# Performance work log

Hardware: AMD Instinct MI355X
Metric: run time of the kernel (lower is better)

Reference implementation:

```python
import jax, jax.numpy as jnp
import numpy as np

EPS = 1e-5
N_HEADS = 12


def _layernorm(x, scale, shift):
    mean = jnp.mean(x, axis=-1, keepdims=True)
    var = jnp.mean((x - mean) ** 2, axis=-1, keepdims=True)
    return scale * (x - mean) / jnp.sqrt(var + EPS) + shift


def setup_inputs() -> dict:
    key = jax.random.key(0)
    ks = jax.random.split(key, 8)
    B, L, D = 4, 1024, 768
    inp = {
        "x": jax.random.normal(ks[0], (B, L, D), jnp.float32),
        "Wq": jax.random.normal(ks[1], (D, D), jnp.float32) * 0.02,
        "Wk": jax.random.normal(ks[2], (D, D), jnp.float32) * 0.02,
        "Wv": jax.random.normal(ks[3], (D, D), jnp.float32) * 0.02,
        "Wo": jax.random.normal(ks[4], (D, D), jnp.float32) * 0.02,
        "bo": jnp.zeros((D,), jnp.float32),
        "scale1": jnp.ones((D,), jnp.float32),
        "shift1": jnp.zeros((D,), jnp.float32),
        "scale2": jnp.ones((D,), jnp.float32),
        "shift2": jnp.zeros((D,), jnp.float32),
        "centers": jax.random.normal(ks[5], (D, D), jnp.float32) * 0.1,  # [num_kernels=D, D]
        "lengthscale": jnp.ones((D,), jnp.float32),
        "Wf": jax.random.normal(ks[6], (D, D), jnp.float32) * 0.02,  # [num_kernels, D]
        "bf": jnp.zeros((D,), jnp.float32),
    }
    return inp


def reference(x, Wq, Wk, Wv, Wo, bo, scale1, shift1, scale2, shift2,
              centers, lengthscale, Wf, bf):
    B, L, D = x.shape
    H = N_HEADS
    hd = D // H

    # --- pre-norm causal MHA + residual ---
    h = _layernorm(x, scale1, shift1)
    q = (h @ Wq).reshape(B, L, H, hd).transpose(0, 2, 1, 3)  # [B,H,L,hd]
    k = (h @ Wk).reshape(B, L, H, hd).transpose(0, 2, 1, 3)
    v = (h @ Wv).reshape(B, L, H, hd).transpose(0, 2, 1, 3)

    scores = jnp.einsum("bhqd,bhkd->bhqk", q, k) / jnp.sqrt(jnp.float32(hd))
    causal = jnp.tril(jnp.ones((L, L), bool))
    scores = jnp.where(causal, scores, -jnp.inf)
    attn = jax.nn.softmax(scores, axis=-1)
    ctx = jnp.einsum("bhqk,bhkd->bhqd", attn, v).transpose(0, 2, 1, 3).reshape(B, L, D)
    x = x + (ctx @ Wo + bo)

    # --- pre-norm RBF-kernel FFN + residual ---
    h = _layernorm(x, scale2, shift2)
    hf = (h / lengthscale).reshape(B * L, D)          # ARD scaling
    cf = centers / lengthscale                        # [K, D]
    sq = (jnp.sum(hf * hf, -1)[:, None]
          + jnp.sum(cf * cf, -1)[None, :]
          - 2.0 * hf @ cf.T)
    K = jnp.exp(-0.5 * jnp.maximum(sq, 0.0))          # [B*L, K]
    ff = (K @ Wf + bf).reshape(B, L, D)
    return x + ff
```

## Files before the change

kernel.cpp:

```cpp
#include <hip/hip_runtime.h>

#define EPS_LN 1e-5f

constexpr int Dm   = 768;
constexpr int Bb   = 4;
constexpr int Ls   = 1024;
constexpr int Hh   = 12;
constexpr int HD   = 64;
constexpr int ROWS = Bb * Ls;
constexpr size_t S = (size_t)ROWS * Dm;
constexpr size_t WSZ = (size_t)Dm * Dm;

typedef __attribute__((ext_vector_type(8))) short bf16x8;
typedef __attribute__((ext_vector_type(4))) float f32x4;
typedef const __attribute__((address_space(1))) unsigned int* gas_p;
typedef __attribute__((address_space(3))) unsigned int* las_p;

__device__ __forceinline__ unsigned short f2bf(float f) {
  unsigned int u = __float_as_uint(f);
  u += 0x7fffu + ((u >> 16) & 1u);
  return (unsigned short)(u >> 16);
}
__device__ __forceinline__ void gl_lds16(const unsigned short* g, unsigned short* l) {
  __builtin_amdgcn_global_load_lds((gas_p)g, (las_p)l, 16, 0, 0);
}

__global__ void __launch_bounds__(256) prep_kernel(
    const float* __restrict__ W0, const float* __restrict__ W1,
    const float* __restrict__ W2, const float* __restrict__ W3,
    const float* __restrict__ W4, unsigned short* __restrict__ wtBase,
    const float* __restrict__ centers, const float* __restrict__ ls,
    unsigned short* __restrict__ cb, float* __restrict__ cn,
    const float* __restrict__ x, const float* __restrict__ scale,
    const float* __restrict__ shift, unsigned short* __restrict__ hb)
{
  __shared__ float smem[64 * 65];
  int bx = blockIdx.x, t = threadIdx.x;
  if (bx < 720) {
    int w = bx / 144, rem = bx - w * 144;
    int ky = rem / 12, nx = rem - ky * 12;
    const float* W = w == 0 ? W0 : w == 1 ? W1 : w == 2 ? W2 : w == 3 ? W3 : W4;
    unsigned short* WT = wtBase + (size_t)w * WSZ;
    int k0 = ky * 64, n0 = nx * 64;
    int c = t & 63, r4 = t >> 6;
    #pragma unroll
    for (int p = 0; p < 16; p++) {
      int r = p * 4 + r4;
      smem[r * 65 + c] = W[(size_t)(k0 + r) * Dm + n0 + c];
    }
    __syncthreads();
    #pragma unroll
    for (int p = 0; p < 16; p++) {
      int r = p * 4 + r4;
      WT[(size_t)(n0 + r) * Dm + k0 + c] = f2bf(smem[c * 65 + r]);
    }
  } else if (bx < 1488) {
    int j = bx - 720;
    float s = 0.f;
    #pragma unroll
    for (int i = 0; i < 3; i++) {
      int k = t + 256 * i;
      float c = centers[(size_t)j * Dm + k] / ls[k];
      cb[(size_t)j * Dm + k] = f2bf(c);
      s += c * c;
    }
    smem[t] = s; __syncthreads();
    for (int o = 128; o > 0; o >>= 1) { if (t < o) smem[t] += smem[t + o]; __syncthreads(); }
    if (t == 0) cn[j] = smem[0];
  } else {
    int row = bx - 1488;
    size_t base = (size_t)row * Dm;
    float v0 = x[base + t], v1 = x[base + t + 256], v2 = x[base + t + 512];
    smem[t] = v0 + v1 + v2; __syncthreads();
    for (int o = 128; o > 0; o >>= 1) { if (t < o) smem[t] += smem[t + o]; __syncthreads(); }
    float mean = smem[0] * (1.0f / Dm);
    __syncthreads();
    float d0 = v0 - mean, d1 = v1 - mean, d2 = v2 - mean;
    smem[t] = d0*d0 + d1*d1 + d2*d2; __syncthreads();
    for (int o = 128; o > 0; o >>= 1) { if (t < o) smem[t] += smem[t + o]; __syncthreads(); }
    float rstd = rsqrtf(smem[0] * (1.0f / Dm) + EPS_LN);
    float dd[3] = {d0, d1, d2};
    #pragma unroll
    for (int i = 0; i < 3; i++) {
      int c = t + 256 * i;
      hb[base + c] = f2bf(scale[c] * dd[i] * rstd + shift[c]);
    }
  }
}

__global__ void __launch_bounds__(256) ln2_kernel(
    const float* __restrict__ xin, const float* __restrict__ scale,
    const float* __restrict__ shift, const float* __restrict__ ls,
    unsigned short* __restrict__ o, float* __restrict__ hn)
{
  int row = blockIdx.x, t = threadIdx.x;
  __shared__ float red[256];
  size_t base = (size_t)row * Dm;
  float v0 = xin[base + t], v1 = xin[base + t + 256], v2 = xin[base + t + 512];
  red[t] = v0 + v1 + v2; __syncthreads();
  for (int oo = 128; oo > 0; oo >>= 1) { if (t < oo) red[t] += red[t + oo]; __syncthreads(); }
  float mean = red[0] * (1.0f / Dm);
  __syncthreads();
  float d0 = v0 - mean, d1 = v1 - mean, d2 = v2 - mean;
  red[t] = d0*d0 + d1*d1 + d2*d2; __syncthreads();
  for (int oo = 128; oo > 0; oo >>= 1) { if (t < oo) red[t] += red[t + oo]; __syncthreads(); }
  float rstd = rsqrtf(red[0] * (1.0f / Dm) + EPS_LN);
  float dd[3] = {d0, d1, d2};
  float hsum = 0.f;
  #pragma unroll
  for (int i = 0; i < 3; i++) {
    int c = t + 256 * i;
    float hv = (scale[c] * dd[i] * rstd + shift[c]) / ls[c];
    o[base + c] = f2bf(hv);
    hsum += hv * hv;
  }
  __syncthreads();
  red[t] = hsum; __syncthreads();
  for (int o2 = 128; o2 > 0; o2 >>= 1) { if (t < o2) red[t] += red[t + o2]; __syncthreads(); }
  if (t == 0) hn[row] = red[0];
}

__global__ void __launch_bounds__(256) gemm_qkv(
    const unsigned short* __restrict__ Abf,
    const unsigned short* __restrict__ wqT,
    const unsigned short* __restrict__ wkT,
    const unsigned short* __restrict__ wvT,
    unsigned short* __restrict__ qb,
    unsigned short* __restrict__ kb,
    unsigned short* __restrict__ vbt)
{
  int m0 = blockIdx.y * 64, n0 = blockIdx.x * 64;
  __shared__ unsigned short sm[4096 + 3 * 4096];
  int tid = threadIdx.x;
  int lane = tid & 63, wave = tid >> 6;
  int quad = lane >> 4, l15 = lane & 15;
  int wr = (wave >> 1) << 5, wc = (wave & 1) << 5;

  f32x4 acc[3][2][2];
  #pragma unroll
  for (int w = 0; w < 3; w++)
    #pragma unroll
    for (int i = 0; i < 2; i++)
      #pragma unroll
      for (int j = 0; j < 2; j++) acc[w][i][j] = (f32x4){0.f, 0.f, 0.f, 0.f};

  const unsigned short* gA = Abf + (size_t)(m0 + (tid >> 2)) * Dm + ((tid & 3) << 3);
  size_t bOff = (size_t)(n0 + (tid >> 2)) * Dm + ((tid & 3) << 3);
  const unsigned short* gB[3] = { wqT + bOff, wkT + bOff, wvT + bOff };

  union Frag { bf16x8 v; ushort4 h[2]; };

  for (int k0 = 0; k0 < Dm; k0 += 64) {
    gl_lds16(gA + k0,      &sm[tid * 8]);
    gl_lds16(gA + k0 + 32, &sm[2048 + tid * 8]);
    #pragma unroll
    for (int w = 0; w < 3; w++) {
      gl_lds16(gB[w] + k0,      &sm[4096 + w * 4096 + tid * 8]);
      gl_lds16(gB[w] + k0 + 32, &sm[4096 + w * 4096 + 2048 + tid * 8]);
    }
    __syncthreads();
    Frag af[2][2];
    #pragma unroll
    for (int kc = 0; kc < 2; kc++)
      #pragma unroll
      for (int mi = 0; mi < 2; mi++)
        af[kc][mi].v = *(const bf16x8*)&sm[kc * 2048 + (wr + mi * 16 + l15) * 32 + quad * 8];
    #pragma unroll
    for (int w = 0; w < 3; w++)
      #pragma unroll
      for (int kc = 0; kc < 2; kc++)
        #pragma unroll
        for (int ni = 0; ni < 2; ni++) {
          Frag bf;
          bf.v = *(const bf16x8*)&sm[4096 + w * 4096 + kc * 2048 + (wc + ni * 16 + l15) * 32 + quad * 8];
          #pragma unroll
          for (int mi = 0; mi < 2; mi++)
            acc[w][mi][ni] = __builtin_amdgcn_mfma_f32_16x16x32_bf16(
                af[kc][mi].v, bf.v, acc[w][mi][ni], 0, 0, 0);
        }
    __syncthreads();
  }

  #pragma unroll
  for (int w = 0; w < 2; w++) {
    unsigned short* ob = w ? kb : qb;
    #pragma unroll
    for (int mi = 0; mi < 2; mi++)
      #pragma unroll
      for (int ni = 0; ni < 2; ni++)
        #pragma unroll
        for (int rg = 0; rg < 4; rg++) {
          int gr = m0 + wr + mi * 16 + quad * 4 + rg;
          int gc = n0 + wc + ni * 16 + l15;
          ob[(size_t)gr * Dm + gc] = f2bf(acc[w][mi][ni][rg]);
        }
  }
  #pragma unroll
  for (int mi = 0; mi < 2; mi++)
    #pragma unroll
    for (int ni = 0; ni < 2; ni++)
      #pragma unroll
      for (int rg = 0; rg < 4; rg++) {
        int rl = wr + mi * 16 + quad * 4 + rg;
        int cl = wc + ni * 16 + l15;
        sm[cl * 72 + rl] = f2bf(acc[2][mi][ni][rg]);
      }
  __syncthreads();
  {
    int d = tid >> 2, c0 = (tid & 3) * 16;
    int b_ = m0 >> 10, keybase = m0 & 1023;
    unsigned short* dst = vbt + ((size_t)((blockIdx.x * 4 + b_) * 64 + d)) * 1024 + keybase + c0;
    #pragma unroll
    for (int i = 0; i < 16; i += 4)
      *(ushort4*)(dst + i) = *(const ushort4*)&sm[d * 72 + c0 + i];
  }
}

template<int MODE>
__global__ void __launch_bounds__(256) gemm64(
    const unsigned short* __restrict__ Abf,
    const unsigned short* __restrict__ BT,
    unsigned short* __restrict__ o0,
    float* __restrict__ outF,
    const float* __restrict__ residF,
    const float* __restrict__ biasF,
    const float* __restrict__ hn,
    const float* __restrict__ cn)
{
  __shared__ unsigned short Asm[2][2048];
  __shared__ unsigned short Bsm[2][2048];
  int tid = threadIdx.x;
  int m0 = blockIdx.y * 64, n0 = blockIdx.x * 64;

  if (MODE >= 2) {
    __shared__ float r2[256];
    float mn = 1e30f;
    for (int i = tid; i < ROWS; i += 256) mn = fminf(mn, hn[i]);
    r2[tid] = mn; __syncthreads();
    for (int o = 128; o > 0; o >>= 1) { if (tid < o) r2[tid] = fminf(r2[tid], r2[tid + o]); __syncthreads(); }
    float hmin = r2[0];
    __syncthreads();
    float mx = 0.f;
    for (int i = tid; i < Dm; i += 256) mx = fmaxf(mx, cn[i]);
    r2[tid] = mx; __syncthreads();
    for (int o = 128; o > 0; o >>= 1) { if (tid < o) r2[tid] = fmaxf(r2[tid], r2[tid + o]); __syncthreads(); }
    float cmax = r2[0];
    float a = sqrtf(hmin), bq = sqrtf(cmax);
    bool allz = (a > bq) && ((a - bq) * (a - bq) > 300.0f);
    if (allz) {
      if (MODE == 2) return;
      int r = m0 + (tid >> 2), c0 = n0 + (tid & 3) * 16;
      size_t idx = (size_t)r * Dm + c0;
      #pragma unroll
      for (int i = 0; i < 16; i += 4) {
        float4 xv = *(const float4*)(residF + idx + i);
        float4 ov;
        ov.x = xv.x + biasF[c0 + i + 0];
        ov.y = xv.y + biasF[c0 + i + 1];
        ov.z = xv.z + biasF[c0 + i + 2];
        ov.w = xv.w + biasF[c0 + i + 3];
        *(float4*)(outF + idx + i) = ov;
      }
      return;
    }
    __syncthreads();
  }

  int lane = tid & 63, wave = tid >> 6;
  int quad = lane >> 4, l15 = lane & 15;
  int wr = (wave >> 1) << 5, wc = (wave & 1) << 5;

  f32x4 acc[2][2];
  #pragma unroll
  for (int i = 0; i < 2; i++)
    #pragma unroll
    for (int j = 0; j < 2; j++) acc[i][j] = (f32x4){0.f, 0.f, 0.f, 0.f};

  const unsigned short* gA = Abf + (size_t)(m0 + (tid >> 2)) * Dm + ((tid & 3) << 3);
  const unsigned short* gB = BT  + (size_t)(n0 + (tid >> 2)) * Dm + ((tid & 3) << 3);

  union Frag { bf16x8 v; ushort4 h[2]; };

  for (int k0 = 0; k0 < Dm; k0 += 64) {
    gl_lds16(gA + k0,      &Asm[0][tid * 8]);
    gl_lds16(gA + k0 + 32, &Asm[1][tid * 8]);
    gl_lds16(gB + k0,      &Bsm[0][tid * 8]);
    gl_lds16(gB + k0 + 32, &Bsm[1][tid * 8]);
    __syncthreads();
    #pragma unroll
    for (int kc = 0; kc < 2; kc++) {
      Frag af[2], bfb[2];
      #pragma unroll
      for (int i = 0; i < 2; i++) {
        af[i].v  = *(const bf16x8*)&Asm[kc][(wr + i * 16 + l15) * 32 + quad * 8];
        bfb[i].v = *(const bf16x8*)&Bsm[kc][(wc + i * 16 + l15) * 32 + quad * 8];
      }
      #pragma unroll
      for (int mi = 0; mi < 2; mi++)
        #pragma unroll
        for (int ni = 0; ni < 2; ni++)
          acc[mi][ni] = __builtin_amdgcn_mfma_f32_16x16x32_bf16(
              af[mi].v, bfb[ni].v, acc[mi][ni], 0, 0, 0);
    }
    __syncthreads();
  }

  #pragma unroll
  for (int mi = 0; mi < 2; mi++)
    #pragma unroll
    for (int ni = 0; ni < 2; ni++)
      #pragma unroll
      for (int rg = 0; rg < 4; rg++) {
        int gr = m0 + wr + mi * 16 + quad * 4 + rg;
        int gc = n0 + wc + ni * 16 + l15;
        size_t idx = (size_t)gr * Dm + gc;
        float v = acc[mi][ni][rg];
        if (MODE == 2) {
          float sq = fmaxf(hn[gr] + cn[gc] - 2.0f * v, 0.f);
          o0[idx] = f2bf(__expf(-0.5f * sq));
        } else {
          outF[idx] = residF[idx] + v + biasF[gc];
        }
      }
}

__global__ void __launch_bounds__(256) attn_flash(
    const unsigned short* __restrict__ q,
    const unsigned short* __restrict__ k,
    const unsigned short* __restrict__ vbt,
    unsigned short* __restrict__ ctx)
{
  int bx = blockIdx.x;
  int qt = (bx & 1) ? (15 - (bx >> 1)) : (bx >> 1);
  int h  = blockIdx.y;
  int b  = blockIdx.z;
  int tid = threadIdx.x;
  int lane = tid & 63, wave = tid >> 6;
  int quad = lane >> 4, l15 = lane & 15;

  __shared__ unsigned short Ks[2][2048];
  __shared__ unsigned short Vt[2][2048];
  __shared__ unsigned short QP[4608];

  size_t baseQK = (size_t)(b * Ls) * Dm + h * HD;
  const unsigned short* gVt = vbt + (size_t)((h * 4 + b) * 64 + (tid >> 2)) * 1024 + ((tid & 3) << 3);

  {
    const unsigned short* gQ = q + baseQK + (size_t)(qt * 64 + (tid >> 2)) * Dm + ((tid & 3) << 3);
    gl_lds16(gQ,      &QP[tid * 8]);
    gl_lds16(gQ + 32, &QP[2048 + tid * 8]);
  }
  __syncthreads();

  union Frag { bf16x8 v; ushort4 h[2]; };
  Frag afq[2];
  #pragma unroll
  for (int kc = 0; kc < 2; kc++)
    afq[kc].v = *(const bf16x8*)&QP[kc * 2048 + (wave * 16 + l15) * 32 + quad * 8];

  f32x4 O[4];
  #pragma unroll
  for (int nj = 0; nj < 4; nj++) O[nj] = (f32x4){0.f, 0.f, 0.f, 0.f};
  float lsum[4] = {0.f, 0.f, 0.f, 0.f};

  const unsigned short* gK = k + baseQK + (size_t)(tid >> 2) * Dm + ((tid & 3) << 3);

  for (int kt = 0; kt <= qt; kt++) {
    gl_lds16(gK + (size_t)(kt * 64) * Dm,      &Ks[0][tid * 8]);
    gl_lds16(gK + (size_t)(kt * 64) * Dm + 32, &Ks[1][tid * 8]);
    gl_lds16(gVt + kt * 64,      &Vt[0][tid * 8]);
    gl_lds16(gVt + kt * 64 + 32, &Vt[1][tid * 8]);
    __syncthreads();

    f32x4 sacc[4];
    #pragma unroll
    for (int ni = 0; ni < 4; ni++) {
      sacc[ni] = (f32x4){0.f, 0.f, 0.f, 0.f};
      #pragma unroll
      for (int kc = 0; kc < 2; kc++) {
        Frag bk;
        bk.v = *(const bf16x8*)&Ks[kc][(ni * 16 + l15) * 32 + quad * 8];
        sacc[ni] = __builtin_amdgcn_mfma_f32_16x16x32_bf16(afq[kc].v, bk.v, sacc[ni], 0, 0, 0);
      }
    }

    if (kt == qt) {
      #pragma unroll
      for (int ni = 0; ni < 4; ni++)
        #pragma unroll
        for (int rg = 0; rg < 4; rg++) {
          int rowl = wave * 16 + quad * 4 + rg;
          int coll = ni * 16 + l15;
          if (coll > rowl) sacc[ni][rg] = -1e30f;
        }
    }

    unsigned short (*Ps)[72] = (unsigned short(*)[72])QP;
    #pragma unroll
    for (int ni = 0; ni < 4; ni++)
      #pragma unroll
      for (int rg = 0; rg < 4; rg++) {
        float p = __expf(sacc[ni][rg] * 0.125f);
        lsum[rg] += p;
        Ps[wave * 16 + quad * 4 + rg][ni * 16 + l15] = f2bf(p);
      }

    Frag ap[2];
    #pragma unroll
    for (int kc = 0; kc < 2; kc++)
      ap[kc].v = *(const bf16x8*)&Ps[wave * 16 + l15][kc * 32 + quad * 8];

    #pragma unroll
    for (int nj = 0; nj < 4; nj++)
      #pragma unroll
      for (int kc = 0; kc < 2; kc++) {
        Frag bv;
        bv.v = *(const bf16x8*)&Vt[kc][(nj * 16 + l15) * 32 + quad * 8];
        O[nj] = __builtin_amdgcn_mfma_f32_16x16x32_bf16(ap[kc].v, bv.v, O[nj], 0, 0, 0);
      }
    __syncthreads();
  }

  float linv[4];
  #pragma unroll
  for (int rg = 0; rg < 4; rg++) {
    float l = lsum[rg];
    #pragma unroll
    for (int m = 1; m < 16; m <<= 1) l += __shfl_xor(l, m, 16);
    linv[rg] = 1.0f / l;
  }
  #pragma unroll
  for (int nj = 0; nj < 4; nj++)
    #pragma unroll
    for (int rg = 0; rg < 4; rg++) {
      int row = qt * 64 + wave * 16 + quad * 4 + rg;
      int col = nj * 16 + l15;
      ctx[baseQK + (size_t)row * Dm + col] = f2bf(O[nj][rg] * linv[rg]);
    }
}

extern "C" void kernel_launch(void* const* d_in, const int* in_sizes, int n_in,
                              void* d_out, int out_size, void* d_ws, size_t ws_size,
                              hipStream_t stream)
{
  const float* x      = (const float*)d_in[0];
  const float* Wq     = (const float*)d_in[1];
  const float* Wk     = (const float*)d_in[2];
  const float* Wv     = (const float*)d_in[3];
  const float* Wo     = (const float*)d_in[4];
  const float* bo     = (const float*)d_in[5];
  const float* scale1 = (const float*)d_in[6];
  const float* shift1 = (const float*)d_in[7];
  const float* scale2 = (const float*)d_in[8];
  const float* shift2 = (const float*)d_in[9];
  const float* centers= (const float*)d_in[10];
  const float* lsp    = (const float*)d_in[11];
  const float* Wf     = (const float*)d_in[12];
  const float* bfv    = (const float*)d_in[13];
  float* out = (float*)d_out;

  unsigned short* wsu = (unsigned short*)d_ws;
  unsigned short* wqT = wsu;
  unsigned short* wkT = wsu + WSZ;
  unsigned short* wvT = wsu + 2 * WSZ;
  unsigned short* woT = wsu + 3 * WSZ;
  unsigned short* wfT = wsu + 4 * WSZ;
  unsigned short* cb  = wsu + 5 * WSZ;
  unsigned short* bufA = wsu + 6 * WSZ;
  unsigned short* bufB = bufA + S;
  unsigned short* hb  = bufA;
  unsigned short* qb  = bufB;
  unsigned short* kb  = bufB + S;
  unsigned short* vbt = bufB + 2 * S;
  unsigned short* ctx = bufA;
  float* x1f          = (float*)bufB;
  unsigned short* hf  = bufB + 2 * S;
  unsigned short* Km  = bufA;
  float* hn = (float*)(bufB + 3 * S);
  float* cn = hn + ROWS;

  dim3 gg(Dm / 64, ROWS / 64);

  prep_kernel<<<5584, 256, 0, stream>>>(Wq, Wk, Wv, Wo, Wf, wsu,
                                        centers, lsp, cb, cn,
                                        x, scale1, shift1, hb);
  gemm_qkv<<<dim3(12, 64), 256, 0, stream>>>(hb, wqT, wkT, wvT, qb, kb, vbt);
  attn_flash<<<dim3(Ls / 64, Hh, Bb), 256, 0, stream>>>(qb, kb, vbt, ctx);
  gemm64<1><<<gg, 256, 0, stream>>>(ctx, woT, nullptr, x1f, x, bo, nullptr, nullptr);
  ln2_kernel<<<ROWS, 256, 0, stream>>>(x1f, scale2, shift2, lsp, hf, hn);
  gemm64<2><<<gg, 256, 0, stream>>>(hf, cb, Km, nullptr, nullptr, nullptr, hn, cn);
  gemm64<3><<<gg, 256, 0, stream>>>(Km, wfT, nullptr, out, x1f, bfv, hn, cn);
}
```

Measured before the change: 190.0 us.

## Use 128x128 MFMA tiles for QKV and output-projection GEMMs

```diff
diff --git a/kernel.cpp b/kernel.cpp
--- a/kernel.cpp
+++ b/kernel.cpp
@@ -120,100 +120,141 @@
   if (t == 0) hn[row] = red[0];
 }
 
-__global__ void __launch_bounds__(256) gemm_qkv(
+__device__ __forceinline__ void gemm128_loop(
     const unsigned short* __restrict__ Abf,
-    const unsigned short* __restrict__ wqT,
-    const unsigned short* __restrict__ wkT,
-    const unsigned short* __restrict__ wvT,
+    const unsigned short* __restrict__ BT,
+    unsigned short* sm, int m0, int n0, int tid, f32x4 (&acc)[4][4])
+{
+  int lane = tid & 63, wave = tid >> 6;
+  int quad = lane >> 4, l15 = lane & 15;
+  int wr = (wave >> 1) << 6, wc = (wave & 1) << 6;
+
+  const unsigned short* gA = Abf + (size_t)(m0 + (tid >> 3)) * Dm + ((tid & 7) << 3);
+  const unsigned short* gB = BT  + (size_t)(n0 + (tid >> 3)) * Dm + ((tid & 7) << 3);
+
+  for (int k0 = 0; k0 < Dm; k0 += 64) {
+    #pragma unroll
+    for (int r = 0; r < 4; r++) {
+      gl_lds16(gA + (size_t)(r * 32) * Dm + k0, &sm[r * 2048 + tid * 8]);
+      gl_lds16(gB + (size_t)(r * 32) * Dm + k0, &sm[8192 + r * 2048 + tid * 8]);
+    }
+    __syncthreads();
+    #pragma unroll
+    for (int kc = 0; kc < 2; kc++) {
+      bf16x8 af[4], bfv[4];
+      #pragma unroll
+      for (int i = 0; i < 4; i++) {
+        af[i]  = *(const bf16x8*)&sm[(wr + i * 16 + l15) * 64 + kc * 32 + quad * 8];
+        bfv[i] = *(const bf16x8*)&sm[8192 + (wc + i * 16 + l15) * 64 + kc * 32 + quad * 8];
+      }
+      #pragma unroll
+      for (int mi = 0; mi < 4; mi++)
+        #pragma unroll
+        for (int ni = 0; ni < 4; ni++)
+          acc[mi][ni] = __builtin_amdgcn_mfma_f32_16x16x32_bf16(af[mi], bfv[ni], acc[mi][ni], 0, 0, 0);
+    }
+    __syncthreads();
+  }
+}
+
+__global__ void __launch_bounds__(256) gemm_qkv128(
+    const unsigned short* __restrict__ Abf,
+    const unsigned short* __restrict__ BT,
     unsigned short* __restrict__ qb,
     unsigned short* __restrict__ kb,
     unsigned short* __restrict__ vbt)
 {
-  int m0 = blockIdx.y * 64, n0 = blockIdx.x * 64;
-  __shared__ unsigned short sm[4096 + 3 * 4096];
+  __shared__ unsigned short sm[18432];
   int tid = threadIdx.x;
+  int m0 = blockIdx.y * 128, n0 = blockIdx.x * 128;
+
+  f32x4 acc[4][4];
+  #pragma unroll
+  for (int i = 0; i < 4; i++)
+    #pragma unroll
+    for (int j = 0; j < 4; j++) acc[i][j] = (f32x4){0.f, 0.f, 0.f, 0.f};
+
+  gemm128_loop(Abf, BT, sm, m0, n0, tid, acc);
+
   int lane = tid & 63, wave = tid >> 6;
   int quad = lane >> 4, l15 = lane & 15;
-  int wr = (wave >> 1) << 5, wc = (wave & 1) << 5;
-
-  f32x4 acc[3][2][2];
-  #pragma unroll
-  for (int w = 0; w < 3; w++)
-    #pragma unroll
-    for (int i = 0; i < 2; i++)
-      #pragma unroll
-      for (int j = 0; j < 2; j++) acc[w][i][j] = (f32x4){0.f, 0.f, 0.f, 0.f};
-
-  const unsigned short* gA = Abf + (size_t)(m0 + (tid >> 2)) * Dm + ((tid & 3) << 3);
-  size_t bOff = (size_t)(n0 + (tid >> 2)) * Dm + ((tid & 3) << 3);
-  const unsigned short* gB[3] = { wqT + bOff, wkT + bOff, wvT + bOff };
-
-  union Frag { bf16x8 v; ushort4 h[2]; };
-
-  for (int k0 = 0; k0 < Dm; k0 += 64) {
-    gl_lds16(gA + k0,      &sm[tid * 8]);
-    gl_lds16(gA + k0 + 32, &sm[2048 + tid * 8]);
-    #pragma unroll
-    for (int w = 0; w < 3; w++) {
-      gl_lds16(gB[w] + k0,      &sm[4096 + w * 4096 + tid * 8]);
-      gl_lds16(gB[w] + k0 + 32, &sm[4096 + w * 4096 + 2048 + tid * 8]);
-    }
-    __syncthreads();
-    Frag af[2][2];
-    #pragma unroll
-    for (int kc = 0; kc < 2; kc++)
-      #pragma unroll
-      for (int mi = 0; mi < 2; mi++)
-        af[kc][mi].v = *(const bf16x8*)&sm[kc * 2048 + (wr + mi * 16 + l15) * 32 + quad * 8];
-    #pragma unroll
-    for (int w = 0; w < 3; w++)
-      #pragma unroll
-      for (int kc = 0; kc < 2; kc++)
-        #pragma unroll
-        for (int ni = 0; ni < 2; ni++) {
-          Frag bf;
-          bf.v = *(const bf16x8*)&sm[4096 + w * 4096 + kc * 2048 + (wc + ni * 16 + l15) * 32 + quad * 8];
-          #pragma unroll
-          for (int mi = 0; mi < 2; mi++)
-            acc[w][mi][ni] = __builtin_amdgcn_mfma_f32_16x16x32_bf16(
-                af[kc][mi].v, bf.v, acc[w][mi][ni], 0, 0, 0);
-        }
-    __syncthreads();
-  }
-
-  #pragma unroll
-  for (int w = 0; w < 2; w++) {
-    unsigned short* ob = w ? kb : qb;
-    #pragma unroll
-    for (int mi = 0; mi < 2; mi++)
-      #pragma unroll
-      for (int ni = 0; ni < 2; ni++)
+  int wr = (wave >> 1) << 6, wc = (wave & 1) << 6;
+
+  if (n0 < 1536) {
+    unsigned short* ob = n0 < 768 ? qb : kb;
+    int nb = n0 < 768 ? n0 : n0 - 768;
+    #pragma unroll
+    for (int mi = 0; mi < 4; mi++)
+      #pragma unroll
+      for (int ni = 0; ni < 4; ni++)
         #pragma unroll
         for (int rg = 0; rg < 4; rg++) {
           int gr = m0 + wr + mi * 16 + quad * 4 + rg;
-          int gc = n0 + wc + ni * 16 + l15;
-          ob[(size_t)gr * Dm + gc] = f2bf(acc[w][mi][ni][rg]);
+          int gc = nb + wc + ni * 16 + l15;
+          ob[(size_t)gr * Dm + gc] = f2bf(acc[mi][ni][rg]);
         }
-  }
-  #pragma unroll
-  for (int mi = 0; mi < 2; mi++)
-    #pragma unroll
-    for (int ni = 0; ni < 2; ni++)
+  } else {
+    unsigned short* tr = sm + wave * 4608;
+    #pragma unroll
+    for (int mi = 0; mi < 4; mi++)
+      #pragma unroll
+      for (int ni = 0; ni < 4; ni++)
+        #pragma unroll
+        for (int rg = 0; rg < 4; rg++) {
+          int rl = mi * 16 + quad * 4 + rg;
+          int cl = ni * 16 + l15;
+          tr[cl * 72 + rl] = f2bf(acc[mi][ni][rg]);
+        }
+    __syncthreads();
+    int b_ = m0 >> 10, key0 = m0 & 1023;
+    int d = tid >> 2, c0 = (tid & 3) << 4;
+    #pragma unroll
+    for (int wq = 0; wq < 4; wq++) {
+      int wrq = (wq >> 1) << 6, wcq = (wq & 1) << 6;
+      int h = ((n0 - 1536) + wcq) >> 6;
+      unsigned short* dst = vbt + ((size_t)((h * 4 + b_) * 64 + d)) * 1024 + key0 + wrq + c0;
+      const unsigned short* srcp = &sm[wq * 4608 + d * 72 + c0];
+      #pragma unroll
+      for (int i = 0; i < 16; i += 4)
+        *(ushort4*)(dst + i) = *(const ushort4*)(srcp + i);
+    }
+  }
+}
+
+__global__ void __launch_bounds__(256) gemm128_out(
+    const unsigned short* __restrict__ Abf,
+    const unsigned short* __restrict__ BT,
+    const float* __restrict__ residF,
+    const float* __restrict__ biasF,
+    float* __restrict__ outF)
+{
+  __shared__ unsigned short sm[16384];
+  int tid = threadIdx.x;
+  int m0 = blockIdx.y * 128, n0 = blockIdx.x * 128;
+
+  f32x4 acc[4][4];
+  #pragma unroll
+  for (int i = 0; i < 4; i++)
+    #pragma unroll
+    for (int j = 0; j < 4; j++) acc[i][j] = (f32x4){0.f, 0.f, 0.f, 0.f};
+
+  gemm128_loop(Abf, BT, sm, m0, n0, tid, acc);
+
+  int lane = tid & 63, wave = tid >> 6;
+  int quad = lane >> 4, l15 = lane & 15;
+  int wr = (wave >> 1) << 6, wc = (wave & 1) << 6;
+
+  #pragma unroll
+  for (int mi = 0; mi < 4; mi++)
+    #pragma unroll
+    for (int ni = 0; ni < 4; ni++)
       #pragma unroll
       for (int rg = 0; rg < 4; rg++) {
-        int rl = wr + mi * 16 + quad * 4 + rg;
-        int cl = wc + ni * 16 + l15;
-        sm[cl * 72 + rl] = f2bf(acc[2][mi][ni][rg]);
-      }
-  __syncthreads();
-  {
-    int d = tid >> 2, c0 = (tid & 3) * 16;
-    int b_ = m0 >> 10, keybase = m0 & 1023;
-    unsigned short* dst = vbt + ((size_t)((blockIdx.x * 4 + b_) * 64 + d)) * 1024 + keybase + c0;
-    #pragma unroll
-    for (int i = 0; i < 16; i += 4)
-      *(ushort4*)(dst + i) = *(const ushort4*)&sm[d * 72 + c0 + i];
-  }
+        int gr = m0 + wr + mi * 16 + quad * 4 + rg;
+        int gc = n0 + wc + ni * 16 + l15;
+        size_t idx = (size_t)gr * Dm + gc;
+        outF[idx] = residF[idx] + acc[mi][ni][rg] + biasF[gc];
+      }
 }
 
 template<int MODE>
@@ -461,7 +502,6 @@
 
   unsigned short* wsu = (unsigned short*)d_ws;
   unsigned short* wqT = wsu;
-  unsigned short* wkT = wsu + WSZ;
   unsigned short* wvT = wsu + 2 * WSZ;
   unsigned short* woT = wsu + 3 * WSZ;
   unsigned short* wfT = wsu + 4 * WSZ;
@@ -484,9 +524,9 @@
   prep_kernel<<<5584, 256, 0, stream>>>(Wq, Wk, Wv, Wo, Wf, wsu,
                                         centers, lsp, cb, cn,
                                         x, scale1, shift1, hb);
-  gemm_qkv<<<dim3(12, 64), 256, 0, stream>>>(hb, wqT, wkT, wvT, qb, kb, vbt);
+  gemm_qkv128<<<dim3(18, 32), 256, 0, stream>>>(hb, wqT, qb, kb, vbt);
   attn_flash<<<dim3(Ls / 64, Hh, Bb), 256, 0, stream>>>(qb, kb, vbt, ctx);
-  gemm64<1><<<gg, 256, 0, stream>>>(ctx, woT, nullptr, x1f, x, bo, nullptr, nullptr);
+  gemm128_out<<<dim3(6, 32), 256, 0, stream>>>(ctx, woT, x, bo, x1f);
   ln2_kernel<<<ROWS, 256, 0, stream>>>(x1f, scale2, shift2, lsp, hf, hn);
   gemm64<2><<<gg, 256, 0, stream>>>(hf, cb, Km, nullptr, nullptr, nullptr, hn, cn);
   gemm64<3><<<gg, 256, 0, stream>>>(Km, wfT, nullptr, out, x1f, bfv, hn, cn);
```

New measurement: 214.9 us. +13.1%, slower.

## Load attention K/V fragments directly from global memory, drop LDS staging

Applied to the files above, without the earlier changes.

```diff
diff --git a/kernel.cpp b/kernel.cpp
--- a/kernel.cpp
+++ b/kernel.cpp
@@ -338,49 +338,33 @@
   int lane = tid & 63, wave = tid >> 6;
   int quad = lane >> 4, l15 = lane & 15;
 
-  __shared__ unsigned short Ks[2][2048];
-  __shared__ unsigned short Vt[2][2048];
-  __shared__ unsigned short QP[4608];
+  __shared__ unsigned short Ps_s[64 * 72];
+  unsigned short (*Ps)[72] = (unsigned short(*)[72])Ps_s;
 
   size_t baseQK = (size_t)(b * Ls) * Dm + h * HD;
-  const unsigned short* gVt = vbt + (size_t)((h * 4 + b) * 64 + (tid >> 2)) * 1024 + ((tid & 3) << 3);
-
-  {
-    const unsigned short* gQ = q + baseQK + (size_t)(qt * 64 + (tid >> 2)) * Dm + ((tid & 3) << 3);
-    gl_lds16(gQ,      &QP[tid * 8]);
-    gl_lds16(gQ + 32, &QP[2048 + tid * 8]);
-  }
-  __syncthreads();
-
-  union Frag { bf16x8 v; ushort4 h[2]; };
-  Frag afq[2];
+
+  bf16x8 afq[2];
   #pragma unroll
   for (int kc = 0; kc < 2; kc++)
-    afq[kc].v = *(const bf16x8*)&QP[kc * 2048 + (wave * 16 + l15) * 32 + quad * 8];
+    afq[kc] = *(const bf16x8*)&q[baseQK + (size_t)(qt * 64 + wave * 16 + l15) * Dm + kc * 32 + quad * 8];
 
   f32x4 O[4];
   #pragma unroll
   for (int nj = 0; nj < 4; nj++) O[nj] = (f32x4){0.f, 0.f, 0.f, 0.f};
   float lsum[4] = {0.f, 0.f, 0.f, 0.f};
 
-  const unsigned short* gK = k + baseQK + (size_t)(tid >> 2) * Dm + ((tid & 3) << 3);
+  const unsigned short* kBase = k + baseQK + (size_t)l15 * Dm + quad * 8;
+  const unsigned short* vBase = vbt + ((size_t)((h * 4 + b) * 64) + l15) * 1024 + quad * 8;
 
   for (int kt = 0; kt <= qt; kt++) {
-    gl_lds16(gK + (size_t)(kt * 64) * Dm,      &Ks[0][tid * 8]);
-    gl_lds16(gK + (size_t)(kt * 64) * Dm + 32, &Ks[1][tid * 8]);
-    gl_lds16(gVt + kt * 64,      &Vt[0][tid * 8]);
-    gl_lds16(gVt + kt * 64 + 32, &Vt[1][tid * 8]);
-    __syncthreads();
-
     f32x4 sacc[4];
     #pragma unroll
     for (int ni = 0; ni < 4; ni++) {
       sacc[ni] = (f32x4){0.f, 0.f, 0.f, 0.f};
       #pragma unroll
       for (int kc = 0; kc < 2; kc++) {
-        Frag bk;
-        bk.v = *(const bf16x8*)&Ks[kc][(ni * 16 + l15) * 32 + quad * 8];
-        sacc[ni] = __builtin_amdgcn_mfma_f32_16x16x32_bf16(afq[kc].v, bk.v, sacc[ni], 0, 0, 0);
+        bf16x8 bk = *(const bf16x8*)&kBase[(size_t)(kt * 64 + ni * 16) * Dm + kc * 32];
+        sacc[ni] = __builtin_amdgcn_mfma_f32_16x16x32_bf16(afq[kc], bk, sacc[ni], 0, 0, 0);
       }
     }
 
@@ -395,7 +379,6 @@
         }
     }
 
-    unsigned short (*Ps)[72] = (unsigned short(*)[72])QP;
     #pragma unroll
     for (int ni = 0; ni < 4; ni++)
       #pragma unroll
@@ -405,20 +388,18 @@
         Ps[wave * 16 + quad * 4 + rg][ni * 16 + l15] = f2bf(p);
       }
 
-    Frag ap[2];
+    bf16x8 ap[2];
     #pragma unroll
     for (int kc = 0; kc < 2; kc++)
-      ap[kc].v = *(const bf16x8*)&Ps[wave * 16 + l15][kc * 32 + quad * 8];
+      ap[kc] = *(const bf16x8*)&Ps[wave * 16 + l15][kc * 32 + quad * 8];
 
     #pragma unroll
     for (int nj = 0; nj < 4; nj++)
       #pragma unroll
       for (int kc = 0; kc < 2; kc++) {
-        Frag bv;
-        bv.v = *(const bf16x8*)&Vt[kc][(nj * 16 + l15) * 32 + quad * 8];
-        O[nj] = __builtin_amdgcn_mfma_f32_16x16x32_bf16(ap[kc].v, bv.v, O[nj], 0, 0, 0);
-      }
-    __syncthreads();
+        bf16x8 bv = *(const bf16x8*)&vBase[(size_t)(nj * 16) * 1024 + kt * 64 + kc * 32];
+        O[nj] = __builtin_amdgcn_mfma_f32_16x16x32_bf16(ap[kc], bv, O[nj], 0, 0, 0);
+      }
   }
 
   float linv[4];
```

Result: slower. 249.1 us (+31.1%).
